# Performance work log

Hardware: AMD Instinct MI355X
Metric: run time of the kernel (lower is better)

## Reference

```python
import jax, jax.numpy as jnp
import numpy as np

EMBED, HEAD, CTX = 1024, 64, 2048

def setup_inputs() -> dict:
    key = jax.random.key(0)
    k1, k2, k3, k4 = jax.random.split(key, 4)
    x = jax.random.normal(k1, (16, 2048, EMBED), dtype=jnp.float32)
    s = EMBED ** -0.5  # torch Linear default init scale-ish
    Wq = jax.random.normal(k2, (EMBED, HEAD), dtype=jnp.float32) * s
    Wk = jax.random.normal(k3, (EMBED, HEAD), dtype=jnp.float32) * s
    Wv = jax.random.normal(k4, (EMBED, HEAD), dtype=jnp.float32) * s
    return {"x": x, "Wq": Wq, "Wk": Wk, "Wv": Wv}

def reference(x, Wq, Wk, Wv):
    # x: [B, S, E] -> q,k,v: [B, S, H]
    q = jnp.einsum('bse,eh->bsh', x, Wq)
    k = jnp.einsum('bse,eh->bsh', x, Wk)
    v = jnp.einsum('bse,eh->bsh', x, Wv)
    scale = k.shape[-1] ** -0.5
    scores = jnp.einsum('bqh,bkh->bqk', q, k) * scale  # [B, S, S]
    S = x.shape[1]
    causal = jnp.tril(jnp.ones((S, S), dtype=bool))
    scores = jnp.where(causal, scores, -jnp.inf)
    attn = jax.nn.softmax(scores, axis=-1)
    return jnp.einsum('bqk,bkh->bqh', attn, v)  # [B, S, H]
```

## Files before the change

kernel.cpp:

```cpp
#include <hip/hip_runtime.h>
#include <math.h>

#define BATCH 16
#define SEQ   2048
#define EMB   1024
#define HD    64
#define NROWS (BATCH*SEQ)

typedef __attribute__((ext_vector_type(8))) short short8;
typedef __attribute__((ext_vector_type(4))) float f32x4;

#define SWZ(byte, row)   ((byte) ^ (((row) & 7) << 4))
#define SWZ16(byte, row) ((byte) ^ (((row) & 15) << 4))

__device__ __forceinline__ ushort f2bf(float f) {
    union { float f; unsigned u; } c; c.f = f;
    return (ushort)((c.u + 0x7FFF + ((c.u >> 16) & 1)) >> 16);
}

__device__ __forceinline__ void gload_lds16(const void* g, void* l) {
    __builtin_amdgcn_global_load_lds(
        (const __attribute__((address_space(1))) void*)g,
        (__attribute__((address_space(3))) void*)l, 16, 0, 0);
}

__global__ void k_transpose_w(const float* __restrict__ Wq,
                              const float* __restrict__ Wk,
                              const float* __restrict__ Wv,
                              ushort* __restrict__ wt) {
    int idx  = blockIdx.x * 256 + threadIdx.x;
    int c192 = idx >> 10;
    int e    = idx & 1023;
    const float* W = (c192 < 64) ? Wq : (c192 < 128 ? Wk : Wv);
    wt[idx] = f2bf(W[e * HD + (c192 & 63)]);
}

__global__ __launch_bounds__(256)
void k_qkv_proj(const float* __restrict__ x, const ushort* __restrict__ wt,
                ushort* __restrict__ qkv, ushort* __restrict__ vt) {
    __shared__ short8 smem[65536 / 16];
    char* base = (char*)smem;
    const int t = threadIdx.x, lane = t & 63, w = t >> 6;
    const int l15 = lane & 15, lg = lane >> 4;
    const int row0 = blockIdx.x * 64;

    f32x4 acc[3][4];
    #pragma unroll
    for (int mi = 0; mi < 3; ++mi)
        #pragma unroll
        for (int n = 0; n < 4; ++n) acc[mi][n] = (f32x4){0.f, 0.f, 0.f, 0.f};

    float4 xr[2][2];

    auto issue_x = [&](int ch) {
        #pragma unroll
        for (int i = 0; i < 2; ++i) {
            int fidx = t + i * 256;
            int r = fidx >> 3, j = fidx & 7;
            const float* src = &x[(size_t)(row0 + r) * EMB + ch * 64 + j * 8];
            xr[i][0] = *(const float4*)(src);
            xr[i][1] = *(const float4*)(src + 4);
        }
    };
    auto write_x = [&](int buf) {
        char* xb = base + buf * 32768;
        #pragma unroll
        for (int i = 0; i < 2; ++i) {
            int fidx = t + i * 256;
            int r = fidx >> 3, j = fidx & 7;
            short8 o;
            o[0] = (short)f2bf(xr[i][0].x); o[1] = (short)f2bf(xr[i][0].y);
            o[2] = (short)f2bf(xr[i][0].z); o[3] = (short)f2bf(xr[i][0].w);
            o[4] = (short)f2bf(xr[i][1].x); o[5] = (short)f2bf(xr[i][1].y);
            o[6] = (short)f2bf(xr[i][1].z); o[7] = (short)f2bf(xr[i][1].w);
            *(short8*)(xb + SWZ(r * 128 + j * 16, r)) = o;
        }
    };
    auto issue_w = [&](int ch, int buf) {
        char* wb = base + buf * 32768 + 8192;
        #pragma unroll
        for (int i = 0; i < 6; ++i) {
            int r = (w * 6 + i) * 8 + (lane >> 3);
            int j = (lane & 7) ^ (r & 7);
            gload_lds16(&wt[(size_t)r * EMB + ch * 64 + j * 8],
                        wb + (w * 6 + i) * 1024);
        }
    };
    auto compute = [&](int buf) {
        char* xb = base + buf * 32768;
        char* wb = base + buf * 32768 + 8192;
        #pragma unroll
        for (int s = 0; s < 2; ++s) {
            short8 xf[4], wf[3];
            #pragma unroll
            for (int n = 0; n < 4; ++n) {
                int r = n * 16 + l15;
                xf[n] = *(short8*)(xb + SWZ(r * 128 + s * 64 + lg * 16, r));
            }
            #pragma unroll
            for (int mi = 0; mi < 3; ++mi) {
                int cr = w * 48 + mi * 16 + l15;
                wf[mi] = *(short8*)(wb + SWZ(cr * 128 + s * 64 + lg * 16, cr));
            }
            __builtin_amdgcn_s_setprio(1);
            #pragma unroll
            for (int mi = 0; mi < 3; ++mi) {
                bool vsec = (w * 48 + mi * 16) >= 128;
                #pragma unroll
                for (int n = 0; n < 4; ++n)
                    acc[mi][n] = vsec
                        ? __builtin_amdgcn_mfma_f32_16x16x32_bf16(xf[n], wf[mi], acc[mi][n], 0, 0, 0)
                        : __builtin_amdgcn_mfma_f32_16x16x32_bf16(wf[mi], xf[n], acc[mi][n], 0, 0, 0);
            }
            __builtin_amdgcn_s_setprio(0);
        }
    };

    issue_x(0); issue_w(0, 0); write_x(0);
    __syncthreads();
    for (int ch = 0; ch < 16; ++ch) {
        int cur = ch & 1, nxt = cur ^ 1;
        if (ch < 15) { issue_w(ch + 1, nxt); issue_x(ch + 1); }
        compute(cur);
        if (ch < 15) write_x(nxt);
        __syncthreads();
    }

    char* qkb = base;
    char* vtb = base + 16384;
    const float qscale = 0.125f * 1.44269504f;
    #pragma unroll
    for (int mi = 0; mi < 3; ++mi) {
        int cg0 = w * 48 + mi * 16;
        bool vsec = cg0 >= 128;
        #pragma unroll
        for (int n = 0; n < 4; ++n) {
            ushort4 o;
            if (!vsec) {
                float sc = (cg0 < 64) ? qscale : 1.0f;
                o.x = f2bf(acc[mi][n][0] * sc); o.y = f2bf(acc[mi][n][1] * sc);
                o.z = f2bf(acc[mi][n][2] * sc); o.w = f2bf(acc[mi][n][3] * sc);
                int xrow = n * 16 + l15, c = cg0 + lg * 4;
                *(ushort4*)(qkb + SWZ16(xrow * 256 + c * 2, xrow)) = o;
            } else {
                o.x = f2bf(acc[mi][n][0]); o.y = f2bf(acc[mi][n][1]);
                o.z = f2bf(acc[mi][n][2]); o.w = f2bf(acc[mi][n][3]);
                int hd = cg0 - 128 + l15, key = n * 16 + lg * 4;
                *(ushort4*)(vtb + SWZ(hd * 128 + key * 2, hd)) = o;
            }
        }
    }
    __syncthreads();
    const int b = row0 >> 11, r0b = row0 & 2047;
    #pragma unroll
    for (int i = 0; i < 4; ++i) {
        int idx = t + i * 256;
        int r = idx >> 4, g = idx & 15;
        short8 v = *(short8*)(qkb + SWZ16(r * 256 + g * 16, r));
        int c0 = g * 8, m = c0 >> 6, c = c0 & 63;
        *(short8*)&qkv[((size_t)m * NROWS + row0 + r) * HD + c] = v;
    }
    #pragma unroll
    for (int i = 0; i < 2; ++i) {
        int idx = t + i * 256;
        int hd = idx >> 3, g = idx & 7;
        short8 v = *(short8*)(vtb + SWZ(hd * 128 + g * 16, hd));
        *(short8*)&vt[((size_t)b * HD + hd) * SEQ + r0b + g * 8] = v;
    }
}

__global__ __launch_bounds__(256)
void k_attn(const ushort* __restrict__ q, const ushort* __restrict__ k,
            const ushort* __restrict__ vt, float* __restrict__ out) {
    __shared__ short8 smem[81920 / 16];
    char* base = (char*)smem;
    char* pls  = base + 65536;
    const int t = threadIdx.x, lane = t & 63, w = t >> 6;
    const int l15 = lane & 15, lg = lane >> 4;
    const int b = blockIdx.x & 15, qt = 31 - (blockIdx.x >> 4);
    const int row0 = qt * 64, r0w = row0 + w * 16;
    const ushort* qb = q  + (size_t)b * SEQ * HD;
    const ushort* kb = k  + (size_t)b * SEQ * HD;
    const ushort* vb = vt + (size_t)b * HD * SEQ;
    char* pw = pls + w * 4096;

    short8 qf[2];
    #pragma unroll
    for (int s = 0; s < 2; ++s)
        qf[s] = *(const short8*)&qb[(size_t)(r0w + l15) * HD + s * 32 + lg * 8];

    f32x4 oacc[4];
    #pragma unroll
    for (int h = 0; h < 4; ++h) oacc[h] = (f32x4){0.f, 0.f, 0.f, 0.f};
    float m_ = -INFINITY, l_ = 0.f;

    auto stage = [&](int kt, int buf) {
        char* kbuf = base + buf * 32768;
        char* vbuf = kbuf + 16384;
        int k0 = kt * 128;
        #pragma unroll
        for (int g = 0; g < 4; ++g) {
            int rk = w * 32 + g * 8 + (lane >> 3);
            int jk = (lane & 7) ^ (rk & 7);
            gload_lds16(&kb[(size_t)(k0 + rk) * HD + jk * 8],
                        kbuf + (w * 4 + g) * 1024);
            int rv = w * 16 + g * 4 + (lane >> 4);
            int jv = (lane & 15) ^ (rv & 15);
            gload_lds16(&vb[(size_t)rv * SEQ + k0 + jv * 8],
                        vbuf + (w * 4 + g) * 1024);
        }
    };

    const int npair = (qt + 2) >> 1;
    stage(0, 0);
    __syncthreads();
    for (int kt = 0; kt < npair; ++kt) {
        int cur = kt & 1;
        if (kt + 1 < npair) stage(kt + 1, cur ^ 1);
        char* kls = base + cur * 32768;
        char* vls = kls + 16384;
        int k0 = kt * 128;

        f32x4 sa[8];
        #pragma unroll
        for (int a = 0; a < 8; ++a) sa[a] = (f32x4){0.f, 0.f, 0.f, 0.f};
        __builtin_amdgcn_s_setprio(1);
        #pragma unroll
        for (int s = 0; s < 2; ++s)
            #pragma unroll
            for (int a = 0; a < 8; ++a) {
                int r = a * 16 + l15;
                short8 kf = *(short8*)(kls + SWZ(r * 128 + s * 64 + lg * 16, r));
                sa[a] = __builtin_amdgcn_mfma_f32_16x16x32_bf16(kf, qf[s], sa[a], 0, 0, 0);
            }
        __builtin_amdgcn_s_setprio(0);

        if (kt == npair - 1) {
            int qrow = r0w + l15;
            #pragma unroll
            for (int a = 0; a < 8; ++a)
                #pragma unroll
                for (int r = 0; r < 4; ++r)
                    if (k0 + a * 16 + lg * 4 + r > qrow) sa[a][r] = -INFINITY;
        }

        float smax = -INFINITY;
        #pragma unroll
        for (int a = 0; a < 8; ++a)
            #pragma unroll
            for (int r = 0; r < 4; ++r) smax = fmaxf(smax, sa[a][r]);
        smax = fmaxf(smax, __shfl_xor(smax, 16));
        smax = fmaxf(smax, __shfl_xor(smax, 32));
        if (!__all(smax - m_ <= 8.0f)) {
            float mn   = fmaxf(m_, smax);
            float corr = __builtin_amdgcn_exp2f(m_ - mn);
            l_ *= corr;
            #pragma unroll
            for (int h = 0; h < 4; ++h) oacc[h] *= corr;
            m_ = mn;
        }
        float p[32], ps = 0.f;
        #pragma unroll
        for (int a = 0; a < 8; ++a)
            #pragma unroll
            for (int r = 0; r < 4; ++r) {
                float pv = __builtin_amdgcn_exp2f(sa[a][r] - m_);
                p[a * 4 + r] = pv; ps += pv;
            }
        ps += __shfl_xor(ps, 16);
        ps += __shfl_xor(ps, 32);
        l_ += ps;

        #pragma unroll
        for (int a = 0; a < 8; ++a) {
            ushort4 pb;
            pb.x = f2bf(p[a * 4 + 0]); pb.y = f2bf(p[a * 4 + 1]);
            pb.z = f2bf(p[a * 4 + 2]); pb.w = f2bf(p[a * 4 + 3]);
            *(ushort4*)(pw + SWZ16(l15 * 256 + a * 32 + lg * 8, l15)) = pb;
        }

        __builtin_amdgcn_s_setprio(1);
        #pragma unroll
        for (int ki = 0; ki < 4; ++ki) {
            short8 pf = *(short8*)(pw + SWZ16(l15 * 256 + ki * 64 + lg * 16, l15));
            #pragma unroll
            for (int h = 0; h < 4; ++h) {
                int rr = h * 16 + l15;
                short8 vf = *(short8*)(vls + SWZ16(rr * 256 + ki * 64 + lg * 16, rr));
                oacc[h] = __builtin_amdgcn_mfma_f32_16x16x32_bf16(vf, pf, oacc[h], 0, 0, 0);
            }
        }
        __builtin_amdgcn_s_setprio(0);
        __syncthreads();
    }

    float inv = 1.0f / l_;
    #pragma unroll
    for (int h = 0; h < 4; ++h) {
        f32x4 v = oacc[h] * inv;
        int qr = w * 16 + l15;
        *(f32x4*)(base + SWZ16(qr * 256 + h * 64 + lg * 16, qr)) = v;
    }
    __syncthreads();
    #pragma unroll
    for (int i = 0; i < 4; ++i) {
        int idx = t + i * 256;
        int r = idx >> 4, g = idx & 15;
        f32x4 v = *(f32x4*)(base + SWZ16(r * 256 + g * 16, r));
        *(f32x4*)&out[((size_t)b * SEQ + row0 + r) * HD + g * 4] = v;
    }
}

extern "C" void kernel_launch(void* const* d_in, const int* in_sizes, int n_in,
                              void* d_out, int out_size, void* d_ws, size_t ws_size,
                              hipStream_t stream) {
    const float* x  = (const float*)d_in[0];
    const float* Wq = (const float*)d_in[1];
    const float* Wk = (const float*)d_in[2];
    const float* Wv = (const float*)d_in[3];
    float* out = (float*)d_out;
    ushort* ws = (ushort*)d_ws;
    ushort* wt16 = ws;
    ushort* qk16 = ws + 192 * 1024;
    ushort* vt16 = qk16 + (size_t)2 * NROWS * HD;

    k_transpose_w<<<768, 256, 0, stream>>>(Wq, Wk, Wv, wt16);
    k_qkv_proj  <<<NROWS / 64, 256, 0, stream>>>(x, wt16, qk16, vt16);
    k_attn      <<<BATCH * (SEQ / 64), 256, 0, stream>>>(
                    qk16, qk16 + (size_t)NROWS * HD, vt16, out);
}
```

Before: 70.42 us.

## Load x fragments directly into registers and repartition QKV projection warps by rows

The QKV projection kernel no longer stages x through LDS. Each wave now owns 16 rows of x and loads its MFMA fragment straight from global memory into registers, converting to bf16 in place. Each wave now computes all 192 output columns for its rows, reading every W fragment from LDS, instead of 48 columns over all 64 rows. This drops the x LDS writes, reads and swizzle and shrinks LDS per block. In exchange, each wave reads four times as much W from LDS and issues strided global loads of x with only one chunk of register prefetch.

```diff
diff --git a/kernel.cpp b/kernel.cpp
--- a/kernel.cpp
+++ b/kernel.cpp
@@ -38,46 +38,21 @@
 __global__ __launch_bounds__(256)
 void k_qkv_proj(const float* __restrict__ x, const ushort* __restrict__ wt,
                 ushort* __restrict__ qkv, ushort* __restrict__ vt) {
-    __shared__ short8 smem[65536 / 16];
+    __shared__ short8 smem[49152 / 16];
     char* base = (char*)smem;
     const int t = threadIdx.x, lane = t & 63, w = t >> 6;
     const int l15 = lane & 15, lg = lane >> 4;
     const int row0 = blockIdx.x * 64;
-
-    f32x4 acc[3][4];
-    #pragma unroll
-    for (int mi = 0; mi < 3; ++mi)
-        #pragma unroll
-        for (int n = 0; n < 4; ++n) acc[mi][n] = (f32x4){0.f, 0.f, 0.f, 0.f};
-
-    float4 xr[2][2];
-
-    auto issue_x = [&](int ch) {
-        #pragma unroll
-        for (int i = 0; i < 2; ++i) {
-            int fidx = t + i * 256;
-            int r = fidx >> 3, j = fidx & 7;
-            const float* src = &x[(size_t)(row0 + r) * EMB + ch * 64 + j * 8];
-            xr[i][0] = *(const float4*)(src);
-            xr[i][1] = *(const float4*)(src + 4);
-        }
-    };
-    auto write_x = [&](int buf) {
-        char* xb = base + buf * 32768;
-        #pragma unroll
-        for (int i = 0; i < 2; ++i) {
-            int fidx = t + i * 256;
-            int r = fidx >> 3, j = fidx & 7;
-            short8 o;
-            o[0] = (short)f2bf(xr[i][0].x); o[1] = (short)f2bf(xr[i][0].y);
-            o[2] = (short)f2bf(xr[i][0].z); o[3] = (short)f2bf(xr[i][0].w);
-            o[4] = (short)f2bf(xr[i][1].x); o[5] = (short)f2bf(xr[i][1].y);
-            o[6] = (short)f2bf(xr[i][1].z); o[7] = (short)f2bf(xr[i][1].w);
-            *(short8*)(xb + SWZ(r * 128 + j * 16, r)) = o;
-        }
-    };
-    auto issue_w = [&](int ch, int buf) {
-        char* wb = base + buf * 32768 + 8192;
+    const float* xrowp = x + (size_t)(row0 + w * 16 + l15) * EMB;
+
+    f32x4 acc[12];
+    #pragma unroll
+    for (int mi = 0; mi < 12; ++mi) acc[mi] = (f32x4){0.f, 0.f, 0.f, 0.f};
+
+    float4 xc[4], xn[4];
+
+    auto stage_w = [&](int ch, int buf) {
+        char* wb = base + buf * 24576;
         #pragma unroll
         for (int i = 0; i < 6; ++i) {
             int r = (w * 6 + i) * 8 + (lane >> 3);
@@ -86,43 +61,42 @@
                         wb + (w * 6 + i) * 1024);
         }
     };
-    auto compute = [&](int buf) {
-        char* xb = base + buf * 32768;
-        char* wb = base + buf * 32768 + 8192;
+    auto load_x = [&](int ch, float4* xr) {
         #pragma unroll
         for (int s = 0; s < 2; ++s) {
-            short8 xf[4], wf[3];
-            #pragma unroll
-            for (int n = 0; n < 4; ++n) {
-                int r = n * 16 + l15;
-                xf[n] = *(short8*)(xb + SWZ(r * 128 + s * 64 + lg * 16, r));
-            }
-            #pragma unroll
-            for (int mi = 0; mi < 3; ++mi) {
-                int cr = w * 48 + mi * 16 + l15;
-                wf[mi] = *(short8*)(wb + SWZ(cr * 128 + s * 64 + lg * 16, cr));
-            }
+            const float* p = xrowp + ch * 64 + s * 32 + lg * 8;
+            xr[s * 2 + 0] = *(const float4*)(p);
+            xr[s * 2 + 1] = *(const float4*)(p + 4);
+        }
+    };
+
+    stage_w(0, 0); load_x(0, xc);
+    __syncthreads();
+    for (int ch = 0; ch < 16; ++ch) {
+        int cur = ch & 1;
+        if (ch < 15) { stage_w(ch + 1, cur ^ 1); load_x(ch + 1, xn); }
+        char* wb = base + cur * 24576;
+        #pragma unroll
+        for (int s = 0; s < 2; ++s) {
+            const float* xp = (const float*)&xc[s * 2];
+            short8 xf;
+            #pragma unroll
+            for (int e = 0; e < 8; ++e) xf[e] = (short)f2bf(xp[e]);
             __builtin_amdgcn_s_setprio(1);
             #pragma unroll
-            for (int mi = 0; mi < 3; ++mi) {
-                bool vsec = (w * 48 + mi * 16) >= 128;
-                #pragma unroll
-                for (int n = 0; n < 4; ++n)
-                    acc[mi][n] = vsec
-                        ? __builtin_amdgcn_mfma_f32_16x16x32_bf16(xf[n], wf[mi], acc[mi][n], 0, 0, 0)
-                        : __builtin_amdgcn_mfma_f32_16x16x32_bf16(wf[mi], xf[n], acc[mi][n], 0, 0, 0);
+            for (int mi = 0; mi < 12; ++mi) {
+                int cr = mi * 16 + l15;
+                short8 wf = *(short8*)(wb + SWZ(cr * 128 + s * 64 + lg * 16, cr));
+                acc[mi] = (mi < 8)
+                    ? __builtin_amdgcn_mfma_f32_16x16x32_bf16(wf, xf, acc[mi], 0, 0, 0)
+                    : __builtin_amdgcn_mfma_f32_16x16x32_bf16(xf, wf, acc[mi], 0, 0, 0);
             }
             __builtin_amdgcn_s_setprio(0);
         }
-    };
-
-    issue_x(0); issue_w(0, 0); write_x(0);
-    __syncthreads();
-    for (int ch = 0; ch < 16; ++ch) {
-        int cur = ch & 1, nxt = cur ^ 1;
-        if (ch < 15) { issue_w(ch + 1, nxt); issue_x(ch + 1); }
-        compute(cur);
-        if (ch < 15) write_x(nxt);
+        if (ch < 15) {
+            #pragma unroll
+            for (int i = 0; i < 4; ++i) xc[i] = xn[i];
+        }
         __syncthreads();
     }
 
@@ -130,24 +104,19 @@
     char* vtb = base + 16384;
     const float qscale = 0.125f * 1.44269504f;
     #pragma unroll
-    for (int mi = 0; mi < 3; ++mi) {
-        int cg0 = w * 48 + mi * 16;
-        bool vsec = cg0 >= 128;
-        #pragma unroll
-        for (int n = 0; n < 4; ++n) {
-            ushort4 o;
-            if (!vsec) {
-                float sc = (cg0 < 64) ? qscale : 1.0f;
-                o.x = f2bf(acc[mi][n][0] * sc); o.y = f2bf(acc[mi][n][1] * sc);
-                o.z = f2bf(acc[mi][n][2] * sc); o.w = f2bf(acc[mi][n][3] * sc);
-                int xrow = n * 16 + l15, c = cg0 + lg * 4;
-                *(ushort4*)(qkb + SWZ16(xrow * 256 + c * 2, xrow)) = o;
-            } else {
-                o.x = f2bf(acc[mi][n][0]); o.y = f2bf(acc[mi][n][1]);
-                o.z = f2bf(acc[mi][n][2]); o.w = f2bf(acc[mi][n][3]);
-                int hd = cg0 - 128 + l15, key = n * 16 + lg * 4;
-                *(ushort4*)(vtb + SWZ(hd * 128 + key * 2, hd)) = o;
-            }
+    for (int mi = 0; mi < 12; ++mi) {
+        ushort4 o;
+        if (mi < 8) {
+            float sc = (mi < 4) ? qscale : 1.0f;
+            o.x = f2bf(acc[mi][0] * sc); o.y = f2bf(acc[mi][1] * sc);
+            o.z = f2bf(acc[mi][2] * sc); o.w = f2bf(acc[mi][3] * sc);
+            int xrow = w * 16 + l15, c = mi * 16 + lg * 4;
+            *(ushort4*)(qkb + SWZ16(xrow * 256 + c * 2, xrow)) = o;
+        } else {
+            o.x = f2bf(acc[mi][0]); o.y = f2bf(acc[mi][1]);
+            o.z = f2bf(acc[mi][2]); o.w = f2bf(acc[mi][3]);
+            int hd = (mi - 8) * 16 + l15, key = w * 16 + lg * 4;
+            *(ushort4*)(vtb + SWZ(hd * 128 + key * 2, hd)) = o;
         }
     }
     __syncthreads();
```

Result: faster. 68.75 us (-2.4%).
